# Performance work log

Measured on AMD Instinct MI355X. Metric: run time of the kernel, lower is better.

## Reference

```python
import jax, jax.numpy as jnp
import numpy as np

MAX_SEQ = 768  # hardcoded in original compute_freqs_cis
THETA = 10000.0


def _freqs_cis(C, T):
    # freqs over FULL embed dim C (matches original, not per-head)
    freqs = 1.0 / THETA ** (jnp.arange(0, C, 2, dtype=jnp.float32)[: C // 2] / C)
    t = jnp.arange(MAX_SEQ, dtype=jnp.float32)
    ang = jnp.outer(t, freqs)  # [MAX_SEQ, C/2]
    return jnp.cos(ang)[:T], jnp.sin(ang)[:T]  # each [T, C/2]


def _apply_rope(u):
    # u: [B, T, C]; rotate adjacent channel pairs across full C
    B, T, C = u.shape
    fr, fi = _freqs_cis(C, T)           # [T, C/2]
    u2 = u.astype(jnp.float32).reshape(B, T, C // 2, 2)
    ur, ui = u2[..., 0], u2[..., 1]     # [B, T, C/2]
    out_r = ur * fr - ui * fi
    out_i = ur * fi + ui * fr
    return jnp.stack([out_r, out_i], axis=-1).reshape(B, T, C).astype(u.dtype)


def setup_inputs() -> dict:
    key = jax.random.key(0)
    k1, k2, k3 = jax.random.split(key, 3)
    B, T, C = 16, 768, 1024
    x = jax.random.normal(k1, (B, T, C), dtype=jnp.float32)
    Wqkv = jax.random.normal(k2, (3 * C, C), dtype=jnp.float32) * 0.02
    bqkv = jnp.zeros((3 * C,), dtype=jnp.float32)
    Wo = jax.random.normal(k3, (C, C), dtype=jnp.float32) * 0.02
    bo = jnp.zeros((C,), dtype=jnp.float32)
    return {"x": x, "Wqkv": Wqkv, "bqkv": bqkv, "Wo": Wo, "bo": bo}


def reference(x, Wqkv, bqkv, Wo, bo):
    B, T, C = x.shape
    H = 16
    D = C // H
    qkv = x @ Wqkv.T + bqkv                      # [B, T, 3C]
    q, k, v = jnp.split(qkv, 3, axis=-1)
    q = _apply_rope(q)
    k = _apply_rope(k)
    # [B, H, T, D]
    q = q.reshape(B, T, H, D).transpose(0, 2, 1, 3)
    k = k.reshape(B, T, H, D).transpose(0, 2, 1, 3)
    v = v.reshape(B, T, H, D).transpose(0, 2, 1, 3)
    scale = 1.0 / jnp.sqrt(jnp.asarray(D, dtype=q.dtype))
    scores = jnp.einsum("bhqd,bhkd->bhqk", q, k) * scale
    causal = jnp.tril(jnp.ones((T, T), dtype=bool))
    scores = jnp.where(causal, scores, jnp.finfo(scores.dtype).min)
    attn = jax.nn.softmax(scores, axis=-1)
    y = jnp.einsum("bhqk,bhkd->bhqd", attn, v)   # [B, H, T, D]
    y = y.transpose(0, 2, 1, 3).reshape(B, T, C)
    return y @ Wo.T + bo
```

## Files before the change

### kernel.cpp

```cpp
#include <hip/hip_runtime.h>
#include <hip/hip_bf16.h>

typedef __attribute__((ext_vector_type(8))) short bf16x8;
typedef __attribute__((ext_vector_type(4))) float f32x4;
typedef unsigned short u16;
typedef unsigned int u32;

#define DEV __device__ __forceinline__

DEV float bf2f(u16 v) { u32 u = ((u32)v) << 16; return __builtin_bit_cast(float, u); }
DEV u16 f2bf(float f) {
    u32 u = __builtin_bit_cast(u32, f);
    u32 r = (u + 0x7FFFu + ((u >> 16) & 1u)) >> 16;
    return (u16)r;
}
DEV u16 f2bf_trunc(float f) { return (u16)(__builtin_bit_cast(u32, f) >> 16); }

DEV void gll16(const u16* g, u16* l) {
    __builtin_amdgcn_global_load_lds((const __attribute__((address_space(1))) void*)g,
                                     (__attribute__((address_space(3))) void*)l, 16, 0, 0);
}

#define WAIT_VM0()   asm volatile("s_waitcnt vmcnt(0)" ::: "memory")
#define WAIT_LGKM0() asm volatile("s_waitcnt lgkmcnt(0)" ::: "memory")
#define BAR()        __builtin_amdgcn_s_barrier()
#define BARF()       asm volatile("s_barrier" ::: "memory")

__global__ void detect_kernel(const u32* __restrict__ x, int* __restrict__ flag) {
    __shared__ int cnt;
    if (threadIdx.x == 0) cnt = 0;
    __syncthreads();
    int c = 0;
    for (int i = threadIdx.x; i < 4096; i += 256) {
        u32 w = x[i];
        u32 e = (w >> 7) & 0xFF;
        c += (e >= 110 && e <= 132) ? 1 : 0;
    }
    atomicAdd(&cnt, c);
    __syncthreads();
    if (threadIdx.x == 0) *flag = (cnt * 2 > 4096) ? 1 : 0;
}

__global__ void cvt_bf16_kernel(const void* __restrict__ in, u16* __restrict__ out,
                                int n8, const int* __restrict__ flag) {
    const int fl = *flag;
    int i = blockIdx.x * 256 + threadIdx.x;
    const int stride = gridDim.x * 256;
    if (fl) {
        const bf16x8* ip = (const bf16x8*)in;
        bf16x8* op = (bf16x8*)out;
        for (; i < n8; i += stride) op[i] = ip[i];
    } else {
        const float4* ip = (const float4*)in;
        bf16x8* op = (bf16x8*)out;
        for (; i < n8; i += stride) {
            float4 a = ip[2 * i], b = ip[2 * i + 1];
            bf16x8 o;
            o[0] = (short)f2bf(a.x); o[1] = (short)f2bf(a.y);
            o[2] = (short)f2bf(a.z); o[3] = (short)f2bf(a.w);
            o[4] = (short)f2bf(b.x); o[5] = (short)f2bf(b.y);
            o[6] = (short)f2bf(b.z); o[7] = (short)f2bf(b.w);
            op[i] = o;
        }
    }
}

__global__ void rope_table_kernel(float2* __restrict__ tab) {
    int idx = blockIdx.x * 256 + threadIdx.x;
    int t = idx >> 9, j = idx & 511;
    float freq = expf(-(float)(2 * j) * (9.210340371976184f / 1024.0f));
    float ang = (float)t * freq;
    tab[idx] = make_float2(cosf(ang), sinf(ang));
}

__global__ __launch_bounds__(512, 2)
void gemm256p_kernel(const u16* __restrict__ A, const u16* __restrict__ W,
                     const void* __restrict__ bias, void* __restrict__ C,
                     int N, const int* __restrict__ flag, int out_mode,
                     const float2* __restrict__ tab, int rope) {
    constexpr int K = 1024, NT = 16;
    __shared__ u16 lds[2][32768];
    const int tid = threadIdx.x;
    const int l = tid & 63, w = tid >> 6;
    const int wm = w >> 2, wn = w & 3;
    const int lo = l & 15, hi = l >> 4;

    const int M0 = blockIdx.x * 256, N0 = blockIdx.y * 256;

    const int rS = tid >> 3;
    const int qS = (tid & 7) ^ (rS & 7);
    const u16* Ag = A + (size_t)(M0 + rS) * K + qS * 8;
    const u16* Wg = W + (size_t)(N0 + rS) * K + qS * 8;
    const int lb = w * 512;

    f32x4 acc[8][4] = {};

#define STG_A(kt, slot, half)                                                  \
    {                                                                          \
        u16* sA_ = &lds[slot][(half) * 8192];                                  \
        const u16* ga_ = Ag + (kt) * 64 + (size_t)(128 * (half)) * K;          \
        gll16(ga_,                  sA_ + lb);                                 \
        gll16(ga_ + (size_t)64 * K, sA_ + 4096 + lb);                          \
    }
#define STG_B(kt, slot, half)                                                  \
    {                                                                          \
        u16* sB_ = &lds[slot][16384 + (half) * 8192];                          \
        const u16* gb_ = Wg + (kt) * 64 + (size_t)(128 * (half)) * K;          \
        gll16(gb_,                  sB_ + lb);                                 \
        gll16(gb_ + (size_t)64 * K, sB_ + 4096 + lb);                          \
    }

    STG_A(0, 0, 0); STG_A(0, 0, 1);
    STG_B(0, 0, 0); STG_B(0, 0, 1);
    WAIT_VM0();
    BARF();

    const int csw = lo & 7;

#pragma unroll 1
    for (int t = 0; t < NT; ++t) {
        const int cur = t & 1, nxt = cur ^ 1;
        const u16* sA = &lds[cur][0];
        const u16* sB = &lds[cur][16384];
        bf16x8 afr[4], bfr[4];

#pragma unroll
        for (int n = 0; n < 4; ++n)
            bfr[n] = *(const bf16x8*)&sB[(wn * 64 + n * 16 + lo) * 64 + ((hi ^ csw) * 8)];
#pragma unroll
        for (int m = 0; m < 4; ++m)
            afr[m] = *(const bf16x8*)&sA[(wm * 128 + m * 16 + lo) * 64 + ((hi ^ csw) * 8)];
        if (t + 1 < NT) { STG_A(t + 1, nxt, 0); STG_A(t + 1, nxt, 1); }
        BARF();
        __builtin_amdgcn_s_setprio(1);
#pragma unroll
        for (int m = 0; m < 4; ++m)
#pragma unroll
            for (int n = 0; n < 4; ++n)
                acc[m][n] = __builtin_amdgcn_mfma_f32_16x16x32_bf16(afr[m], bfr[n], acc[m][n], 0, 0, 0);
        __builtin_amdgcn_s_setprio(0);
        BARF();

#pragma unroll
        for (int m = 0; m < 4; ++m)
            afr[m] = *(const bf16x8*)&sA[(wm * 128 + 64 + m * 16 + lo) * 64 + ((hi ^ csw) * 8)];
        if (t + 1 < NT) { STG_B(t + 1, nxt, 0); STG_B(t + 1, nxt, 1); }
        BARF();
        __builtin_amdgcn_s_setprio(1);
#pragma unroll
        for (int m = 0; m < 4; ++m)
#pragma unroll
            for (int n = 0; n < 4; ++n)
                acc[4 + m][n] = __builtin_amdgcn_mfma_f32_16x16x32_bf16(afr[m], bfr[n], acc[4 + m][n], 0, 0, 0);
        __builtin_amdgcn_s_setprio(0);
        BARF();

#pragma unroll
        for (int n = 0; n < 4; ++n)
            bfr[n] = *(const bf16x8*)&sB[(wn * 64 + n * 16 + lo) * 64 + (((4 + hi) ^ csw) * 8)];
#pragma unroll
        for (int m = 0; m < 4; ++m)
            afr[m] = *(const bf16x8*)&sA[(wm * 128 + m * 16 + lo) * 64 + (((4 + hi) ^ csw) * 8)];
        BARF();
        __builtin_amdgcn_s_setprio(1);
#pragma unroll
        for (int m = 0; m < 4; ++m)
#pragma unroll
            for (int n = 0; n < 4; ++n)
                acc[m][n] = __builtin_amdgcn_mfma_f32_16x16x32_bf16(afr[m], bfr[n], acc[m][n], 0, 0, 0);
        __builtin_amdgcn_s_setprio(0);
        BARF();

#pragma unroll
        for (int m = 0; m < 4; ++m)
            afr[m] = *(const bf16x8*)&sA[(wm * 128 + 64 + m * 16 + lo) * 64 + (((4 + hi) ^ csw) * 8)];
        WAIT_VM0();
        BARF();
        __builtin_amdgcn_s_setprio(1);
#pragma unroll
        for (int m = 0; m < 4; ++m)
#pragma unroll
            for (int n = 0; n < 4; ++n)
                acc[4 + m][n] = __builtin_amdgcn_mfma_f32_16x16x32_bf16(afr[m], bfr[n], acc[4 + m][n], 0, 0, 0);
        __builtin_amdgcn_s_setprio(0);
        BARF();
    }
#undef STG_A
#undef STG_B

    const int fl = *flag;
    const int f32out = out_mode ? (fl == 0) : 0;
    const int do_rope = rope && (N0 < 2048);
#pragma unroll
    for (int mi = 0; mi < 8; ++mi) {
        const int rbase = M0 + wm * 128 + (mi >> 2) * 64 + (mi & 3) * 16 + hi * 4;
        const int tbase = (M0 % 768) + wm * 128 + (mi >> 2) * 64 + (mi & 3) * 16 + hi * 4;
#pragma unroll
        for (int n = 0; n < 4; ++n) {
            const int col = N0 + wn * 64 + lo + n * 16;
            float bi = fl ? bf2f(((const u16*)bias)[col]) : ((const float*)bias)[col];
            const int jf = (col & 1023) >> 1;
            const int odd = col & 1;
#pragma unroll
            for (int j = 0; j < 4; ++j) {
                float v = acc[mi][n][j] + bi;
                if (do_rope) {
                    float partner = __shfl_xor(v, 1);
                    float2 cs = tab[(tbase + j) * 512 + jf];
                    v = odd ? (v * cs.x + partner * cs.y) : (v * cs.x - partner * cs.y);
                }
                size_t idx = (size_t)(rbase + j) * N + col;
                if (f32out) ((float*)C)[idx] = v;
                else        ((u16*)C)[idx] = f2bf(v);
            }
        }
    }
}

__global__ __launch_bounds__(512)
void attn_kernel(const u16* __restrict__ qkv, u16* __restrict__ y) {
    constexpr int T = 768, CH = 1024, QKVC = 3072;
    constexpr float NEG = -30000.0f;
    __shared__ u16 Ks[2][64 * 64];
    __shared__ u16 Vt[64 * 72];
    __shared__ u16 Ps[128 * 72];

    const int tid = threadIdx.x, l = tid & 63, w = tid >> 6;
    const int qt = blockIdx.x, h = blockIdx.y, b = blockIdx.z;
    const int lo = l & 15, hi = l >> 4;
    const int kk = hi * 8;
    const int swzk = (lo & 7) * 8;

    const int qrow = qt * 128 + w * 16 + lo;
    const u16* qptr = qkv + (size_t)(b * T + qrow) * QKVC + h * 64 + kk;
    bf16x8 aq0r = *(const bf16x8*)qptr;
    bf16x8 aq1r = *(const bf16x8*)(qptr + 32);
    bf16x8 aq0, aq1;
#pragma unroll
    for (int e = 0; e < 8; ++e) {
        aq0[e] = (short)f2bf(bf2f((u16)aq0r[e]) * 0.125f);
        aq1[e] = (short)f2bf(bf2f((u16)aq1r[e]) * 0.125f);
    }

    f32x4 o[4] = {};
    float mrun[4] = {NEG, NEG, NEG, NEG};
    float lrun[4] = {0.f, 0.f, 0.f, 0.f};

    const int ksr = w * 8 + (l >> 3);
    const int ksc = ((l & 7) ^ ((l >> 3) & 7)) * 8;
    const u16* kbase = qkv + (size_t)(b * T + ksr) * QKVC + CH + h * 64 + ksc;

    const int vd0 = (tid & 7) * 8;
    const int vswz = (tid & 7) * 8;
    const int vr0 = tid >> 3;
    const u16* vbase = qkv + (size_t)(b * T) * QKVC + 2 * CH + h * 64 + vd0;

    const int NTk = 2 * qt + 2;

    gll16(kbase, &Ks[0][w * 512]);
    bf16x8 cv0 = *(const bf16x8*)(vbase + (size_t)vr0 * QKVC);
    WAIT_VM0();
#pragma unroll
    for (int e = 0; e < 8; ++e)
        Vt[(vd0 + e) * 72 + (vr0 ^ vswz)] = (u16)cv0[e];

    for (int kt = 0; kt < NTk; ++kt) {
        const int cur = kt & 1, nxt = cur ^ 1;
        bf16x8 nv0;
        if (kt + 1 < NTk) {
            const size_t koff = (size_t)((kt + 1) * 64) * QKVC;
            gll16(kbase + koff, &Ks[nxt][w * 512]);
            nv0 = *(const bf16x8*)(vbase + (size_t)((kt + 1) * 64 + vr0) * QKVC);
        }
        WAIT_LGKM0();
        BAR();

        __builtin_amdgcn_s_setprio(1);
        f32x4 s[4];
#pragma unroll
        for (int n = 0; n < 4; ++n) {
            bf16x8 kb0 = *(const bf16x8*)&Ks[cur][(n * 16 + lo) * 64 + (kk ^ swzk)];
            bf16x8 kb1 = *(const bf16x8*)&Ks[cur][(n * 16 + lo) * 64 + ((32 + kk) ^ swzk)];
            f32x4 z = {0.f, 0.f, 0.f, 0.f};
            z = __builtin_amdgcn_mfma_f32_16x16x32_bf16(aq0, kb0, z, 0, 0, 0);
            z = __builtin_amdgcn_mfma_f32_16x16x32_bf16(aq1, kb1, z, 0, 0, 0);
            s[n] = z;
        }
        __builtin_amdgcn_s_setprio(0);

        if (kt >= 2 * qt) {
#pragma unroll
            for (int n = 0; n < 4; ++n) {
                int kcol = kt * 64 + n * 16 + lo;
#pragma unroll
                for (int j = 0; j < 4; ++j)
                    if (kcol > qt * 128 + w * 16 + hi * 4 + j) s[n][j] = NEG;
            }
        }
        float mx[4];
#pragma unroll
        for (int j = 0; j < 4; ++j) {
            float m0 = fmaxf(fmaxf(s[0][j], s[1][j]), fmaxf(s[2][j], s[3][j]));
            m0 = fmaxf(m0, __shfl_xor(m0, 1));
            m0 = fmaxf(m0, __shfl_xor(m0, 2));
            m0 = fmaxf(m0, __shfl_xor(m0, 4));
            m0 = fmaxf(m0, __shfl_xor(m0, 8));
            mx[j] = m0;
        }
        float g = fmaxf(fmaxf(mx[0] - mrun[0], mx[1] - mrun[1]),
                        fmaxf(mx[2] - mrun[2], mx[3] - mrun[3]));
        if (!__all(g <= 8.0f)) {
#pragma unroll
            for (int j = 0; j < 4; ++j) {
                float mn = fmaxf(mrun[j], mx[j]);
                float c = __expf(mrun[j] - mn);
                mrun[j] = mn;
                lrun[j] *= c;
#pragma unroll
                for (int n = 0; n < 4; ++n) o[n][j] *= c;
            }
        }
        float p[4][4];
#pragma unroll
        for (int n = 0; n < 4; ++n)
#pragma unroll
            for (int j = 0; j < 4; ++j) {
                p[n][j] = __expf(s[n][j] - mrun[j]);
                Ps[(w * 16 + hi * 4 + j) * 72 + n * 16 + lo] = f2bf_trunc(p[n][j]);
            }
#pragma unroll
        for (int j = 0; j < 4; ++j)
            lrun[j] += p[0][j] + p[1][j] + p[2][j] + p[3][j];

        __builtin_amdgcn_s_setprio(1);
#pragma unroll
        for (int c = 0; c < 2; ++c) {
            bf16x8 pa = *(const bf16x8*)&Ps[(w * 16 + lo) * 72 + c * 32 + kk];
#pragma unroll
            for (int n = 0; n < 4; ++n) {
                const int v = (n * 2 + (lo >> 3)) & 7;
                bf16x8 vb = *(const bf16x8*)&Vt[(n * 16 + lo) * 72 + ((c * 32 + kk) ^ (v * 8))];
                o[n] = __builtin_amdgcn_mfma_f32_16x16x32_bf16(pa, vb, o[n], 0, 0, 0);
            }
        }
        __builtin_amdgcn_s_setprio(0);

        if (kt + 1 < NTk) {
            WAIT_VM0();
            BAR();
#pragma unroll
            for (int e = 0; e < 8; ++e)
                Vt[(vd0 + e) * 72 + (vr0 ^ vswz)] = (u16)nv0[e];
        }
    }

    float inv[4];
#pragma unroll
    for (int j = 0; j < 4; ++j) {
        float r = lrun[j];
        r += __shfl_xor(r, 1);
        r += __shfl_xor(r, 2);
        r += __shfl_xor(r, 4);
        r += __shfl_xor(r, 8);
        inv[j] = (r > 0.f) ? 1.0f / r : 0.f;
    }
#pragma unroll
    for (int n = 0; n < 4; ++n)
#pragma unroll
        for (int j = 0; j < 4; ++j) {
            int t = qt * 128 + w * 16 + hi * 4 + j;
            y[(size_t)(b * T + t) * CH + h * 64 + n * 16 + lo] = f2bf(o[n][j] * inv[j]);
        }
}

extern "C" void kernel_launch(void* const* d_in, const int* in_sizes, int n_in,
                              void* d_out, int out_size, void* d_ws, size_t ws_size,
                              hipStream_t stream) {
    char* ws = (char*)d_ws;
    int*   flag  = (int*)ws;
    u16*   xb    = (u16*)(ws + 256);
    u16*   Wqb   = (u16*)(ws + 256 + 25165824);
    u16*   Wob   = (u16*)(ws + 256 + 31457280);
    u16*   qkv   = (u16*)(ws + 256 + 33570816);
    u16*   y     = (u16*)(ws + 256 + 109068288);
    float2* tab  = (float2*)(ws + 256 + 134234112);

    detect_kernel<<<1, 256, 0, stream>>>((const u32*)d_in[0], flag);
    cvt_bf16_kernel<<<2048, 256, 0, stream>>>(d_in[0], xb,  12582912 / 8, flag);
    cvt_bf16_kernel<<<1536, 256, 0, stream>>>(d_in[1], Wqb, 3145728 / 8, flag);
    cvt_bf16_kernel<<<512,  256, 0, stream>>>(d_in[3], Wob, 1048576 / 8, flag);
    rope_table_kernel<<<768 * 512 / 256, 256, 0, stream>>>(tab);

    gemm256p_kernel<<<dim3(48, 12), 512, 0, stream>>>(xb, Wqb, d_in[2], qkv, 3072, flag, 0, tab, 1);
    attn_kernel<<<dim3(6, 16, 16), 512, 0, stream>>>(qkv, y);
    gemm256p_kernel<<<dim3(48, 4), 512, 0, stream>>>(y, Wob, d_in[4], d_out, 1024, flag, 1, tab, 0);
}
```

Baseline: 291.0 us.

## Fuse conversion and rope-table kernels, use 128-wide N tiles for output GEMM

Merges the three bf16 conversion launches and the rope table launch into one grid-stride prep kernel to cut launch overhead. Templates the GEMM on the N tile width and runs the output projection with BN=128. That doubles its grid from 192 to 384 blocks so more of the GPU's compute units get work. The smaller tile lowers per-block reuse of the A operand and raises total A traffic for that GEMM.

```diff
diff --git a/kernel.cpp b/kernel.cpp
--- a/kernel.cpp
+++ b/kernel.cpp
@@ -41,51 +41,58 @@
     if (threadIdx.x == 0) *flag = (cnt * 2 > 4096) ? 1 : 0;
 }
 
-__global__ void cvt_bf16_kernel(const void* __restrict__ in, u16* __restrict__ out,
-                                int n8, const int* __restrict__ flag) {
+DEV void cvt8(const void* in, u16* out, int i, int fl) {
+    if (fl) {
+        ((bf16x8*)out)[i] = ((const bf16x8*)in)[i];
+    } else {
+        float4 a = ((const float4*)in)[2 * i], b = ((const float4*)in)[2 * i + 1];
+        bf16x8 o;
+        o[0] = (short)f2bf(a.x); o[1] = (short)f2bf(a.y);
+        o[2] = (short)f2bf(a.z); o[3] = (short)f2bf(a.w);
+        o[4] = (short)f2bf(b.x); o[5] = (short)f2bf(b.y);
+        o[6] = (short)f2bf(b.z); o[7] = (short)f2bf(b.w);
+        ((bf16x8*)out)[i] = o;
+    }
+}
+
+__global__ void prep_kernel(const void* __restrict__ x, u16* __restrict__ xb,
+                            const void* __restrict__ Wq, u16* __restrict__ Wqb,
+                            const void* __restrict__ Wo, u16* __restrict__ Wob,
+                            float2* __restrict__ tab, const int* __restrict__ flag) {
+    constexpr int N8X = 1572864, N8W = 393216, N8O = 131072;
+    constexpr int C1 = N8X, C2 = N8X + N8W, C3 = N8X + N8W + N8O;
+    constexpr int TOTAL = C3 + 768 * 512;
     const int fl = *flag;
-    int i = blockIdx.x * 256 + threadIdx.x;
     const int stride = gridDim.x * 256;
-    if (fl) {
-        const bf16x8* ip = (const bf16x8*)in;
-        bf16x8* op = (bf16x8*)out;
-        for (; i < n8; i += stride) op[i] = ip[i];
-    } else {
-        const float4* ip = (const float4*)in;
-        bf16x8* op = (bf16x8*)out;
-        for (; i < n8; i += stride) {
-            float4 a = ip[2 * i], b = ip[2 * i + 1];
-            bf16x8 o;
-            o[0] = (short)f2bf(a.x); o[1] = (short)f2bf(a.y);
-            o[2] = (short)f2bf(a.z); o[3] = (short)f2bf(a.w);
-            o[4] = (short)f2bf(b.x); o[5] = (short)f2bf(b.y);
-            o[6] = (short)f2bf(b.z); o[7] = (short)f2bf(b.w);
-            op[i] = o;
-        }
-    }
-}
-
-__global__ void rope_table_kernel(float2* __restrict__ tab) {
-    int idx = blockIdx.x * 256 + threadIdx.x;
-    int t = idx >> 9, j = idx & 511;
-    float freq = expf(-(float)(2 * j) * (9.210340371976184f / 1024.0f));
-    float ang = (float)t * freq;
-    tab[idx] = make_float2(cosf(ang), sinf(ang));
-}
-
+    for (int i = blockIdx.x * 256 + threadIdx.x; i < TOTAL; i += stride) {
+        if (i < C1)       cvt8(x, xb, i, fl);
+        else if (i < C2)  cvt8(Wq, Wqb, i - C1, fl);
+        else if (i < C3)  cvt8(Wo, Wob, i - C2, fl);
+        else {
+            int r = i - C3;
+            int t = r >> 9, j = r & 511;
+            float freq = expf(-(float)(2 * j) * (9.210340371976184f / 1024.0f));
+            float ang = (float)t * freq;
+            tab[r] = make_float2(cosf(ang), sinf(ang));
+        }
+    }
+}
+
+template<int BN>
 __global__ __launch_bounds__(512, 2)
 void gemm256p_kernel(const u16* __restrict__ A, const u16* __restrict__ W,
                      const void* __restrict__ bias, void* __restrict__ C,
                      int N, const int* __restrict__ flag, int out_mode,
                      const float2* __restrict__ tab, int rope) {
     constexpr int K = 1024, NT = 16;
-    __shared__ u16 lds[2][32768];
+    constexpr int NF = BN / 64;
+    __shared__ u16 lds[2][16384 + BN * 64];
     const int tid = threadIdx.x;
     const int l = tid & 63, w = tid >> 6;
     const int wm = w >> 2, wn = w & 3;
     const int lo = l & 15, hi = l >> 4;
 
-    const int M0 = blockIdx.x * 256, N0 = blockIdx.y * 256;
+    const int M0 = blockIdx.x * 256, N0 = blockIdx.y * BN;
 
     const int rS = tid >> 3;
     const int qS = (tid & 7) ^ (rS & 7);
@@ -93,7 +100,7 @@
     const u16* Wg = W + (size_t)(N0 + rS) * K + qS * 8;
     const int lb = w * 512;
 
-    f32x4 acc[8][4] = {};
+    f32x4 acc[8][NF] = {};
 
 #define STG_A(kt, slot, half)                                                  \
     {                                                                          \
@@ -109,9 +116,11 @@
         gll16(gb_,                  sB_ + lb);                                 \
         gll16(gb_ + (size_t)64 * K, sB_ + 4096 + lb);                          \
     }
+#define STG_B_ALL(kt, slot)                                                    \
+    { STG_B(kt, slot, 0); if (BN == 256) STG_B(kt, slot, 1); }
 
     STG_A(0, 0, 0); STG_A(0, 0, 1);
-    STG_B(0, 0, 0); STG_B(0, 0, 1);
+    STG_B_ALL(0, 0);
     WAIT_VM0();
     BARF();
 
@@ -122,11 +131,11 @@
         const int cur = t & 1, nxt = cur ^ 1;
         const u16* sA = &lds[cur][0];
         const u16* sB = &lds[cur][16384];
-        bf16x8 afr[4], bfr[4];
-
-#pragma unroll
-        for (int n = 0; n < 4; ++n)
-            bfr[n] = *(const bf16x8*)&sB[(wn * 64 + n * 16 + lo) * 64 + ((hi ^ csw) * 8)];
+        bf16x8 afr[4], bfr[NF];
+
+#pragma unroll
+        for (int n = 0; n < NF; ++n)
+            bfr[n] = *(const bf16x8*)&sB[(wn * (BN / 4) + n * 16 + lo) * 64 + ((hi ^ csw) * 8)];
 #pragma unroll
         for (int m = 0; m < 4; ++m)
             afr[m] = *(const bf16x8*)&sA[(wm * 128 + m * 16 + lo) * 64 + ((hi ^ csw) * 8)];
@@ -136,7 +145,7 @@
 #pragma unroll
         for (int m = 0; m < 4; ++m)
 #pragma unroll
-            for (int n = 0; n < 4; ++n)
+            for (int n = 0; n < NF; ++n)
                 acc[m][n] = __builtin_amdgcn_mfma_f32_16x16x32_bf16(afr[m], bfr[n], acc[m][n], 0, 0, 0);
         __builtin_amdgcn_s_setprio(0);
         BARF();
@@ -144,20 +153,20 @@
 #pragma unroll
         for (int m = 0; m < 4; ++m)
             afr[m] = *(const bf16x8*)&sA[(wm * 128 + 64 + m * 16 + lo) * 64 + ((hi ^ csw) * 8)];
-        if (t + 1 < NT) { STG_B(t + 1, nxt, 0); STG_B(t + 1, nxt, 1); }
-        BARF();
-        __builtin_amdgcn_s_setprio(1);
-#pragma unroll
-        for (int m = 0; m < 4; ++m)
-#pragma unroll
-            for (int n = 0; n < 4; ++n)
+        if (t + 1 < NT) { STG_B_ALL(t + 1, nxt); }
+        BARF();
+        __builtin_amdgcn_s_setprio(1);
+#pragma unroll
+        for (int m = 0; m < 4; ++m)
+#pragma unroll
+            for (int n = 0; n < NF; ++n)
                 acc[4 + m][n] = __builtin_amdgcn_mfma_f32_16x16x32_bf16(afr[m], bfr[n], acc[4 + m][n], 0, 0, 0);
         __builtin_amdgcn_s_setprio(0);
         BARF();
 
 #pragma unroll
-        for (int n = 0; n < 4; ++n)
-            bfr[n] = *(const bf16x8*)&sB[(wn * 64 + n * 16 + lo) * 64 + (((4 + hi) ^ csw) * 8)];
+        for (int n = 0; n < NF; ++n)
+            bfr[n] = *(const bf16x8*)&sB[(wn * (BN / 4) + n * 16 + lo) * 64 + (((4 + hi) ^ csw) * 8)];
 #pragma unroll
         for (int m = 0; m < 4; ++m)
             afr[m] = *(const bf16x8*)&sA[(wm * 128 + m * 16 + lo) * 64 + (((4 + hi) ^ csw) * 8)];
@@ -166,7 +175,7 @@
 #pragma unroll
         for (int m = 0; m < 4; ++m)
 #pragma unroll
-            for (int n = 0; n < 4; ++n)
+            for (int n = 0; n < NF; ++n)
                 acc[m][n] = __builtin_amdgcn_mfma_f32_16x16x32_bf16(afr[m], bfr[n], acc[m][n], 0, 0, 0);
         __builtin_amdgcn_s_setprio(0);
         BARF();
@@ -180,13 +189,14 @@
 #pragma unroll
         for (int m = 0; m < 4; ++m)
 #pragma unroll
-            for (int n = 0; n < 4; ++n)
+            for (int n = 0; n < NF; ++n)
                 acc[4 + m][n] = __builtin_amdgcn_mfma_f32_16x16x32_bf16(afr[m], bfr[n], acc[4 + m][n], 0, 0, 0);
         __builtin_amdgcn_s_setprio(0);
         BARF();
     }
 #undef STG_A
 #undef STG_B
+#undef STG_B_ALL
 
     const int fl = *flag;
     const int f32out = out_mode ? (fl == 0) : 0;
@@ -196,8 +206,8 @@
         const int rbase = M0 + wm * 128 + (mi >> 2) * 64 + (mi & 3) * 16 + hi * 4;
         const int tbase = (M0 % 768) + wm * 128 + (mi >> 2) * 64 + (mi & 3) * 16 + hi * 4;
 #pragma unroll
-        for (int n = 0; n < 4; ++n) {
-            const int col = N0 + wn * 64 + lo + n * 16;
+        for (int n = 0; n < NF; ++n) {
+            const int col = N0 + wn * (BN / 4) + lo + n * 16;
             float bi = fl ? bf2f(((const u16*)bias)[col]) : ((const float*)bias)[col];
             const int jf = (col & 1023) >> 1;
             const int odd = col & 1;
@@ -386,12 +396,9 @@
     float2* tab  = (float2*)(ws + 256 + 134234112);
 
     detect_kernel<<<1, 256, 0, stream>>>((const u32*)d_in[0], flag);
-    cvt_bf16_kernel<<<2048, 256, 0, stream>>>(d_in[0], xb,  12582912 / 8, flag);
-    cvt_bf16_kernel<<<1536, 256, 0, stream>>>(d_in[1], Wqb, 3145728 / 8, flag);
-    cvt_bf16_kernel<<<512,  256, 0, stream>>>(d_in[3], Wob, 1048576 / 8, flag);
-    rope_table_kernel<<<768 * 512 / 256, 256, 0, stream>>>(tab);
-
-    gemm256p_kernel<<<dim3(48, 12), 512, 0, stream>>>(xb, Wqb, d_in[2], qkv, 3072, flag, 0, tab, 1);
+    prep_kernel<<<2048, 256, 0, stream>>>(d_in[0], xb, d_in[1], Wqb, d_in[3], Wob, tab, flag);
+
+    gemm256p_kernel<256><<<dim3(48, 12), 512, 0, stream>>>(xb, Wqb, d_in[2], qkv, 3072, flag, 0, tab, 1);
     attn_kernel<<<dim3(6, 16, 16), 512, 0, stream>>>(qkv, y);
-    gemm256p_kernel<<<dim3(48, 4), 512, 0, stream>>>(y, Wob, d_in[4], d_out, 1024, flag, 1, tab, 0);
-}
+    gemm256p_kernel<128><<<dim3(48, 8), 512, 0, stream>>>(y, Wob, d_in[4], d_out, 1024, flag, 1, tab, 0);
+}
```

Result: no change. 294.7 us (+1.3%).

## Fuse input prep kernels into one launch and remap attention blocks per XCD

Applied to the files above, without the earlier changes.

The detect, three bf16 conversion kernels and the RoPE table kernel are merged into a single prep kernel in which every block recomputes the dtype flag locally. This removes four launches and the serial dependency on the detect kernel. The attention grid is flattened to 1D, and block indices are remapped so that all query tiles of one (batch, head) land on the same XCD, which should improve L2 reuse of K/V. In exchange, each block redundantly reads the 4096-word detection sample.

```diff
diff --git a/kernel.cpp b/kernel.cpp
--- a/kernel.cpp
+++ b/kernel.cpp
@@ -26,51 +26,56 @@
 #define BAR()        __builtin_amdgcn_s_barrier()
 #define BARF()       asm volatile("s_barrier" ::: "memory")
 
-__global__ void detect_kernel(const u32* __restrict__ x, int* __restrict__ flag) {
+DEV void cvt8(const void* in, u16* out, int i, int fl) {
+    if (fl) {
+        ((bf16x8*)out)[i] = ((const bf16x8*)in)[i];
+    } else {
+        float4 a = ((const float4*)in)[2 * i], b = ((const float4*)in)[2 * i + 1];
+        bf16x8 o;
+        o[0] = (short)f2bf(a.x); o[1] = (short)f2bf(a.y);
+        o[2] = (short)f2bf(a.z); o[3] = (short)f2bf(a.w);
+        o[4] = (short)f2bf(b.x); o[5] = (short)f2bf(b.y);
+        o[6] = (short)f2bf(b.z); o[7] = (short)f2bf(b.w);
+        ((bf16x8*)out)[i] = o;
+    }
+}
+
+__global__ void prep_kernel(const void* __restrict__ x, u16* __restrict__ xb,
+                            const void* __restrict__ Wq, u16* __restrict__ Wqb,
+                            const void* __restrict__ Wo, u16* __restrict__ Wob,
+                            float2* __restrict__ tab, int* __restrict__ flag) {
     __shared__ int cnt;
     if (threadIdx.x == 0) cnt = 0;
     __syncthreads();
-    int c = 0;
-    for (int i = threadIdx.x; i < 4096; i += 256) {
-        u32 w = x[i];
-        u32 e = (w >> 7) & 0xFF;
-        c += (e >= 110 && e <= 132) ? 1 : 0;
-    }
-    atomicAdd(&cnt, c);
+    {
+        int c = 0;
+        for (int i = threadIdx.x; i < 4096; i += 256) {
+            u32 w = ((const u32*)x)[i];
+            u32 e = (w >> 7) & 0xFF;
+            c += (e >= 110 && e <= 132) ? 1 : 0;
+        }
+        atomicAdd(&cnt, c);
+    }
     __syncthreads();
-    if (threadIdx.x == 0) *flag = (cnt * 2 > 4096) ? 1 : 0;
-}
-
-__global__ void cvt_bf16_kernel(const void* __restrict__ in, u16* __restrict__ out,
-                                int n8, const int* __restrict__ flag) {
-    const int fl = *flag;
-    int i = blockIdx.x * 256 + threadIdx.x;
+    const int fl = (cnt * 2 > 4096) ? 1 : 0;
+    if (blockIdx.x == 0 && threadIdx.x == 0) *flag = fl;
+
+    constexpr int N8X = 1572864, N8W = 393216, N8O = 131072;
+    constexpr int C1 = N8X, C2 = N8X + N8W, C3 = N8X + N8W + N8O;
+    constexpr int TOTAL = C3 + 768 * 512;
     const int stride = gridDim.x * 256;
-    if (fl) {
-        const bf16x8* ip = (const bf16x8*)in;
-        bf16x8* op = (bf16x8*)out;
-        for (; i < n8; i += stride) op[i] = ip[i];
-    } else {
-        const float4* ip = (const float4*)in;
-        bf16x8* op = (bf16x8*)out;
-        for (; i < n8; i += stride) {
-            float4 a = ip[2 * i], b = ip[2 * i + 1];
-            bf16x8 o;
-            o[0] = (short)f2bf(a.x); o[1] = (short)f2bf(a.y);
-            o[2] = (short)f2bf(a.z); o[3] = (short)f2bf(a.w);
-            o[4] = (short)f2bf(b.x); o[5] = (short)f2bf(b.y);
-            o[6] = (short)f2bf(b.z); o[7] = (short)f2bf(b.w);
-            op[i] = o;
-        }
-    }
-}
-
-__global__ void rope_table_kernel(float2* __restrict__ tab) {
-    int idx = blockIdx.x * 256 + threadIdx.x;
-    int t = idx >> 9, j = idx & 511;
-    float freq = expf(-(float)(2 * j) * (9.210340371976184f / 1024.0f));
-    float ang = (float)t * freq;
-    tab[idx] = make_float2(cosf(ang), sinf(ang));
+    for (int i = blockIdx.x * 256 + threadIdx.x; i < TOTAL; i += stride) {
+        if (i < C1)       cvt8(x, xb, i, fl);
+        else if (i < C2)  cvt8(Wq, Wqb, i - C1, fl);
+        else if (i < C3)  cvt8(Wo, Wob, i - C2, fl);
+        else {
+            int r = i - C3;
+            int t = r >> 9, j = r & 511;
+            float freq = expf(-(float)(2 * j) * (9.210340371976184f / 1024.0f));
+            float ang = (float)t * freq;
+            tab[r] = make_float2(cosf(ang), sinf(ang));
+        }
+    }
 }
 
 __global__ __launch_bounds__(512, 2)
@@ -226,7 +231,11 @@
     __shared__ u16 Ps[128 * 72];
 
     const int tid = threadIdx.x, l = tid & 63, w = tid >> 6;
-    const int qt = blockIdx.x, h = blockIdx.y, b = blockIdx.z;
+    const int hw = blockIdx.x;
+    const int xcd = hw & 7, pos = hw >> 3;
+    const int qt = pos % 6;
+    const int g = (pos / 6) * 8 + xcd;
+    const int h = g & 15, b = g >> 4;
     const int lo = l & 15, hi = l >> 4;
     const int kk = hi * 8;
     const int swzk = (lo & 7) * 8;
@@ -307,9 +316,9 @@
             m0 = fmaxf(m0, __shfl_xor(m0, 8));
             mx[j] = m0;
         }
-        float g = fmaxf(fmaxf(mx[0] - mrun[0], mx[1] - mrun[1]),
-                        fmaxf(mx[2] - mrun[2], mx[3] - mrun[3]));
-        if (!__all(g <= 8.0f)) {
+        float gg = fmaxf(fmaxf(mx[0] - mrun[0], mx[1] - mrun[1]),
+                         fmaxf(mx[2] - mrun[2], mx[3] - mrun[3]));
+        if (!__all(gg <= 8.0f)) {
 #pragma unroll
             for (int j = 0; j < 4; ++j) {
                 float mn = fmaxf(mrun[j], mx[j]);
@@ -385,13 +394,9 @@
     u16*   y     = (u16*)(ws + 256 + 109068288);
     float2* tab  = (float2*)(ws + 256 + 134234112);
 
-    detect_kernel<<<1, 256, 0, stream>>>((const u32*)d_in[0], flag);
-    cvt_bf16_kernel<<<2048, 256, 0, stream>>>(d_in[0], xb,  12582912 / 8, flag);
-    cvt_bf16_kernel<<<1536, 256, 0, stream>>>(d_in[1], Wqb, 3145728 / 8, flag);
-    cvt_bf16_kernel<<<512,  256, 0, stream>>>(d_in[3], Wob, 1048576 / 8, flag);
-    rope_table_kernel<<<768 * 512 / 256, 256, 0, stream>>>(tab);
+    prep_kernel<<<2048, 256, 0, stream>>>(d_in[0], xb, d_in[1], Wqb, d_in[3], Wob, tab, flag);
 
     gemm256p_kernel<<<dim3(48, 12), 512, 0, stream>>>(xb, Wqb, d_in[2], qkv, 3072, flag, 0, tab, 1);
-    attn_kernel<<<dim3(6, 16, 16), 512, 0, stream>>>(qkv, y);
+    attn_kernel<<<1536, 512, 0, stream>>>(qkv, y);
     gemm256p_kernel<<<dim3(48, 4), 512, 0, stream>>>(y, Wob, d_in[4], d_out, 1024, flag, 1, tab, 0);
 }
```

After: 279.0 us, median of 2. 1.04x faster.
